# Performance work log

Hardware: AMD Instinct MI355X
Metric: run time of the kernel (lower is better)

## Reference

```python
import jax, jax.numpy as jnp
import numpy as np

NUM_ENT = 100000
NUM_REL = 50
NUM_EDGES = 200000
NNZ = 1000000
D = 128
BATCH = 4096
C = 1.0  # curvature k of the Lorentz manifold


def lorentz_linear(x, W, b, scale_param):
    # HyboNet-style LorentzLinear: linear map, then rescale so output lies on hyperboloid
    x = x @ W.T + b                                   # [N, D]
    time = jax.nn.sigmoid(x[..., :1]) * jnp.exp(scale_param) + 1.1   # [N, 1]
    xs = x[..., 1:]
    sqnorm = jnp.clip(jnp.sum(xs * xs, axis=-1, keepdims=True), 1e-8, None)
    s = jnp.sqrt((time * time - 1.0) / sqnorm)
    return jnp.concatenate([time, xs * s], axis=-1)


def logmap0(x, k):
    # Lorentz log map at the origin: time component -> 0, spatial rescaled by arccosh distance
    sqrtK = jnp.sqrt(jnp.asarray(k, x.dtype))
    y = x[..., 1:]
    y_norm = jnp.clip(jnp.linalg.norm(y, axis=-1, keepdims=True), 1e-8, None)
    theta = jnp.clip(x[..., :1] / sqrtK, 1.0 + 1e-7, None)
    spatial = sqrtK * jnp.arccosh(theta) * y / y_norm
    return jnp.concatenate([jnp.zeros_like(x[..., :1]), spatial], axis=-1)


def h2conv(X, emb_ty, vertex, edges, ty, lin_W, lin_b, lin_scale, eps):
    N = X.shape[0]
    Xl = lorentz_linear(X, lin_W, lin_b, lin_scale)           # [N, D]
    Xve = Xl[vertex] - emb_ty[ty]                             # [nnz, D] gather - relation translation
    Xe = jax.ops.segment_sum(Xve, edges, num_segments=NUM_EDGES)  # [E, D]
    Xev = Xe[edges]                                           # [nnz, D]
    Xv = jax.ops.segment_sum(Xev, vertex, num_segments=N)     # [N, D]
    return eps * Xv + Xl


def setup_inputs():
    key = jax.random.key(0)
    ks = jax.random.split(key, 20)
    n_ty = (NUM_REL - 1) * 6
    return {
        "emb_E": jax.random.normal(ks[0], (NUM_ENT, D), jnp.float32),
        "emb_R": jax.random.normal(ks[1], (NUM_REL, D), jnp.float32),
        "emb_ty": jax.random.normal(ks[2], (n_ty, D), jnp.float32),
        "lin_W": jax.random.normal(ks[3], (D, D), jnp.float32) * (1.0 / np.sqrt(D)),
        "lin_b": jnp.zeros((D,), jnp.float32),
        "lin_scale": jnp.asarray(np.log(10.0), jnp.float32),
        "eps": jnp.asarray([0.5], jnp.float32),
        "ms": jax.random.uniform(ks[4], (BATCH, 6), dtype=jnp.float32),
        "r_idx": jax.random.randint(ks[5], (BATCH,), 0, NUM_REL),
        "e1_idx": jax.random.randint(ks[6], (BATCH,), 0, NUM_ENT),
        "e2_idx": jax.random.randint(ks[7], (BATCH,), 0, NUM_ENT),
        "e3_idx": jax.random.randint(ks[8], (BATCH,), 0, NUM_ENT),
        "e4_idx": jax.random.randint(ks[9], (BATCH,), 0, NUM_ENT),
        "e5_idx": jax.random.randint(ks[10], (BATCH,), 0, NUM_ENT),
        "e6_idx": jax.random.randint(ks[11], (BATCH,), 0, NUM_ENT),
        "vertex": jax.random.randint(ks[12], (NNZ,), 0, NUM_ENT),
        "edges": jax.random.randint(ks[13], (NNZ,), 0, NUM_EDGES),
        "ty": jax.random.randint(ks[14], (NNZ,), 0, n_ty),
        "bs": BATCH,
    }


def reference(emb_E, emb_R, emb_ty, lin_W, lin_b, lin_scale, eps, ms,
              r_idx, e1_idx, e2_idx, e3_idx, e4_idx, e5_idx, e6_idx,
              vertex, edges, ty, bs):
    # (expmap0 result in the torch code is immediately overwritten, so omitted)
    E_e = h2conv(emb_E, emb_ty, vertex, edges, ty, lin_W, lin_b, lin_scale, eps)
    E_e = logmap0(E_e, C)
    E_e = E_e.at[0].set(1.0)
    R_e = emb_R.at[0].set(1.0)
    r = R_e[r_idx]
    x = (E_e[e1_idx] * E_e[e2_idx] * E_e[e3_idx] *
         E_e[e4_idx] * E_e[e5_idx] * E_e[e6_idx] * r)   # [B, D]
    return jnp.sum(x, axis=1)
```

## Files before the change

kernel.cpp:

```cpp
#include <hip/hip_runtime.h>
#include <math.h>

#define NUM_ENT   100000
#define NUM_REL   50
#define NUM_EDGES 200000
#define NNZ       1000000
#define DIM       128
#define BATCH     4096

#define CAP_E 32
#define CAP_V 40

#define XL_OFF  0
#define XH_OFF  (NUM_ENT * DIM)
#define XE_ROWS 150000
#define XE_OFF  (XH_OFF + NUM_ENT * DIM / 2)
#define INT_OFF (XE_OFF + XE_ROWS * DIM)

#define CUR_E   0
#define CUR_V   (CUR_E + NUM_EDGES)
#define BMV_O   (CUR_V + NUM_ENT)
#define FLAGE_O (BMV_O + 3136)
#define NV_CNT  (FLAGE_O + 50000)
#define NE_CNT  (NV_CNT + 1)
#define ZERO_N  (NE_CNT + 1)
#define VLIST   (ZERO_N)
#define ELIST   (VLIST + 24704)
#define EINV    (ELIST + NUM_EDGES)
#define PAYE    (EINV + NUM_EDGES)
#define PAYV    (PAYE + NUM_EDGES * CAP_E)
#define WSPHI   (PAYV + NUM_ENT * CAP_V)
#define WSPLO   (WSPHI + 8192)

#define FILL8_BLOCKS  489
#define ELIST4_BLOCKS 196
#define FLAGE8_BLOCKS 489
#define GEMM_TILES    1563
#define GF_GRID       2084

typedef __attribute__((ext_vector_type(8))) short sh8;
typedef __attribute__((ext_vector_type(4))) short sh4;
typedef __attribute__((ext_vector_type(4))) float f32x4;
typedef __attribute__((ext_vector_type(4))) _Float16 h4f;

__device__ __forceinline__ int bmtest(const unsigned* __restrict__ bm, int v) {
    return (bm[v >> 5] >> (v & 31)) & 1u;
}

__device__ __forceinline__ void split1(float x, unsigned short& h, unsigned short& l) {
    __bf16 hb = (__bf16)x;
    float hf = (float)hb;
    __bf16 lb = (__bf16)(x - hf);
    h = __builtin_bit_cast(unsigned short, hb);
    l = __builtin_bit_cast(unsigned short, lb);
}

__global__ __launch_bounds__(256, 4) void k_gemm_flage(const float* __restrict__ X,
                                                       const unsigned short* __restrict__ WhiG,
                                                       const unsigned short* __restrict__ WloG,
                                                       const float* __restrict__ bias,
                                                       const float* __restrict__ scale_p,
                                                       float* __restrict__ Y,
                                                       _Float16* __restrict__ Yh,
                                                       const unsigned* __restrict__ bmv,
                                                       const int* __restrict__ edges,
                                                       const int* __restrict__ vertex,
                                                       unsigned char* __restrict__ flag_e) {
    const int bid = blockIdx.x;
    const int sub = bid & 3, grp = bid >> 2;
    const int t = threadIdx.x;

    if (sub == 3) {
        if (grp >= FLAGE8_BLOCKS) return;
        int i8 = (grp * 256 + t) * 8;
        if (i8 >= NNZ) return;
        int4 v0 = *(const int4*)&vertex[i8];
        int4 v1 = *(const int4*)&vertex[i8 + 4];
        int4 e0 = *(const int4*)&edges[i8];
        int4 e1 = *(const int4*)&edges[i8 + 4];
        if (bmtest(bmv, v0.x)) flag_e[e0.x] = 1;
        if (bmtest(bmv, v0.y)) flag_e[e0.y] = 1;
        if (bmtest(bmv, v0.z)) flag_e[e0.z] = 1;
        if (bmtest(bmv, v0.w)) flag_e[e0.w] = 1;
        if (bmtest(bmv, v1.x)) flag_e[e1.x] = 1;
        if (bmtest(bmv, v1.y)) flag_e[e1.y] = 1;
        if (bmtest(bmv, v1.z)) flag_e[e1.z] = 1;
        if (bmtest(bmv, v1.w)) flag_e[e1.w] = 1;
        return;
    }

    __shared__ unsigned short Ahi[64 * 40], Alo[64 * 40];
    __shared__ unsigned short Bhi[128 * 40], Blo[128 * 40];
    __shared__ float biasS[128];

    const int tile = grp * 3 + sub;
    const int row0 = tile * 64;
    const int lane = t & 63, wv = t >> 6;
    const int cq = lane & 15, qd = lane >> 4;
    const float4* X4 = (const float4*)X;

    if (t < 128) biasS[t] = bias[t];

    f32x4 acc[8];
#pragma unroll
    for (int tn = 0; tn < 8; ++tn) acc[tn] = (f32x4){0.f, 0.f, 0.f, 0.f};

    for (int kc = 0; kc < 4; ++kc) {
#pragma unroll
        for (int i = 0; i < 2; ++i) {
            int q = t + 256 * i;
            int row = q >> 3, k4 = q & 7;
            int gr = row0 + row;
            float4 xv = make_float4(0.f, 0.f, 0.f, 0.f);
            if (gr < NUM_ENT) xv = X4[gr * 32 + kc * 8 + k4];
            unsigned short h0, h1, h2, h3, l0, l1, l2, l3;
            split1(xv.x, h0, l0); split1(xv.y, h1, l1);
            split1(xv.z, h2, l2); split1(xv.w, h3, l3);
            *(sh4*)&Ahi[row * 40 + k4 * 4] = (sh4){(short)h0, (short)h1, (short)h2, (short)h3};
            *(sh4*)&Alo[row * 40 + k4 * 4] = (sh4){(short)l0, (short)l1, (short)l2, (short)l3};
        }
#pragma unroll
        for (int i = 0; i < 4; ++i) {
            int q = t + 256 * i;
            int wr = q >> 3, k4 = q & 7;
            *(sh4*)&Bhi[wr * 40 + k4 * 4] =
                *(const sh4*)&WhiG[wr * 128 + kc * 32 + k4 * 4];
            *(sh4*)&Blo[wr * 40 + k4 * 4] =
                *(const sh4*)&WloG[wr * 128 + kc * 32 + k4 * 4];
        }
        __syncthreads();

        sh8 ah = *(const sh8*)&Ahi[(wv * 16 + cq) * 40 + qd * 8];
        sh8 al = *(const sh8*)&Alo[(wv * 16 + cq) * 40 + qd * 8];
#pragma unroll
        for (int tn = 0; tn < 8; ++tn) {
            sh8 bh = *(const sh8*)&Bhi[(tn * 16 + cq) * 40 + qd * 8];
            sh8 bl = *(const sh8*)&Blo[(tn * 16 + cq) * 40 + qd * 8];
            acc[tn] = __builtin_amdgcn_mfma_f32_16x16x32_bf16(ah, bh, acc[tn], 0, 0, 0);
            acc[tn] = __builtin_amdgcn_mfma_f32_16x16x32_bf16(ah, bl, acc[tn], 0, 0, 0);
            acc[tn] = __builtin_amdgcn_mfma_f32_16x16x32_bf16(al, bh, acc[tn], 0, 0, 0);
        }
        __syncthreads();
    }

    float es = expf(scale_p[0]);
    float psum[4] = {0.f, 0.f, 0.f, 0.f};
#pragma unroll
    for (int tn = 0; tn < 8; ++tn) {
        float bj = biasS[tn * 16 + cq];
#pragma unroll
        for (int reg = 0; reg < 4; ++reg) {
            float y = acc[tn][reg] + bj;
            acc[tn][reg] = y;
            psum[reg] += y * y;
        }
    }
#pragma unroll
    for (int off = 1; off < 16; off <<= 1) {
#pragma unroll
        for (int reg = 0; reg < 4; ++reg)
            psum[reg] += __shfl_xor(psum[reg], off, 64);
    }
    float srow[4], trow[4];
#pragma unroll
    for (int reg = 0; reg < 4; ++reg) {
        float y0 = __shfl(acc[0][reg], lane & 48, 64);
        float time = es / (1.f + expf(-y0)) + 1.1f;
        float ps = fmaxf(psum[reg] - y0 * y0, 1e-8f);
        srow[reg] = sqrtf((time * time - 1.f) / ps);
        trow[reg] = time;
    }
    int growv[4], fl[4];
#pragma unroll
    for (int reg = 0; reg < 4; ++reg) {
        int grow = row0 + wv * 16 + qd * 4 + reg;
        growv[reg] = grow;
        fl[reg] = (grow < NUM_ENT) ? bmtest(bmv, grow) : 0;
    }
#pragma unroll
    for (int tn = 0; tn < 8; ++tn) {
        int col = tn * 16 + cq;
#pragma unroll
        for (int reg = 0; reg < 4; ++reg) {
            if (growv[reg] < NUM_ENT) {
                float y = acc[tn][reg];
                float val = (col == 0) ? trow[reg] : y * srow[reg];
                Yh[growv[reg] * 128 + col] = (_Float16)val;
                if (fl[reg]) Y[growv[reg] * 128 + col] = val;
            }
        }
    }
}

__global__ __launch_bounds__(256) void k_flagv(const int* __restrict__ e1,
                                               const int* __restrict__ e2,
                                               const int* __restrict__ e3,
                                               const int* __restrict__ e4,
                                               const int* __restrict__ e5,
                                               const int* __restrict__ e6,
                                               unsigned* __restrict__ bmv,
                                               int* __restrict__ vlist,
                                               int* __restrict__ nv,
                                               const float* __restrict__ W,
                                               unsigned short* __restrict__ Whi,
                                               unsigned short* __restrict__ Wlo) {
    if (blockIdx.x >= 16) {
        int i = (blockIdx.x - 16) * 256 + threadIdx.x;
        unsigned short h, l;
        split1(W[i], h, l);
        Whi[i] = h; Wlo[i] = l;
        return;
    }
    int i = blockIdx.x * 256 + threadIdx.x;
    if (i >= BATCH) return;
    int idx[6] = {e1[i], e2[i], e3[i], e4[i], e5[i], e6[i]};
#pragma unroll
    for (int k = 0; k < 6; ++k) {
        int v = idx[k];
        unsigned bit = 1u << (v & 31);
        unsigned old = atomicOr(&bmv[v >> 5], bit);
        if (!(old & bit))
            vlist[atomicAdd(nv, 1)] = v;
    }
}

__global__ __launch_bounds__(256) void k_fill(const int* __restrict__ edges,
                                              const int* __restrict__ vertex,
                                              const int* __restrict__ tyi,
                                              const unsigned char* __restrict__ flag_e,
                                              const unsigned* __restrict__ bmv,
                                              int* __restrict__ cur_e,
                                              int* __restrict__ cur_v,
                                              int* __restrict__ pay_e,
                                              int* __restrict__ pay_v,
                                              int* __restrict__ elist,
                                              int* __restrict__ einv,
                                              int* __restrict__ ne) {
    int bid = blockIdx.x;
    if (bid >= FILL8_BLOCKS) {
        int i4 = ((bid - FILL8_BLOCKS) * 256 + threadIdx.x) * 4;
        if (i4 >= NUM_EDGES) return;
        int f[4], cnt = 0;
#pragma unroll
        for (int k = 0; k < 4; ++k) {
            int i = i4 + k;
            f[k] = (i < NUM_EDGES) ? flag_e[i] : 0;
            cnt += f[k];
        }
        if (cnt) {
            int g = atomicAdd(ne, cnt);
#pragma unroll
            for (int k = 0; k < 4; ++k) {
                if (f[k]) {
                    elist[g] = i4 + k;
                    einv[i4 + k] = g;
                    ++g;
                }
            }
        }
        return;
    }
    int i8 = (bid * 256 + threadIdx.x) * 8;
    if (i8 >= NNZ) return;
    int vv[8], ee[8], tt[8], nit;
    if (i8 + 7 < NNZ) {
        int4 v0 = *(const int4*)&vertex[i8];
        int4 v1 = *(const int4*)&vertex[i8 + 4];
        int4 e0 = *(const int4*)&edges[i8];
        int4 e1 = *(const int4*)&edges[i8 + 4];
        int4 t0 = *(const int4*)&tyi[i8];
        int4 t1 = *(const int4*)&tyi[i8 + 4];
        vv[0] = v0.x; vv[1] = v0.y; vv[2] = v0.z; vv[3] = v0.w;
        vv[4] = v1.x; vv[5] = v1.y; vv[6] = v1.z; vv[7] = v1.w;
        ee[0] = e0.x; ee[1] = e0.y; ee[2] = e0.z; ee[3] = e0.w;
        ee[4] = e1.x; ee[5] = e1.y; ee[6] = e1.z; ee[7] = e1.w;
        tt[0] = t0.x; tt[1] = t0.y; tt[2] = t0.z; tt[3] = t0.w;
        tt[4] = t1.x; tt[5] = t1.y; tt[6] = t1.z; tt[7] = t1.w;
        nit = 8;
    } else {
        nit = NNZ - i8;
        for (int k = 0; k < nit; ++k) {
            vv[k] = vertex[i8 + k]; ee[k] = edges[i8 + k]; tt[k] = tyi[i8 + k];
        }
    }
#pragma unroll 8
    for (int k = 0; k < nit; ++k) {
        int v = vv[k], e = ee[k];
        if (flag_e[e]) {
            int p = atomicAdd(&cur_e[e], 1);
            if (p < CAP_E) pay_e[e * CAP_E + p] = (v << 9) | tt[k];
        }
        if (bmtest(bmv, v)) {
            int q = atomicAdd(&cur_v[v], 1);
            if (q < CAP_V) pay_v[v * CAP_V + q] = e;
        }
    }
}

__global__ __launch_bounds__(256) void k_gatherE(const _Float16* __restrict__ Xlh,
                                                 const float* __restrict__ Ty,
                                                 const int* __restrict__ elist,
                                                 const int* __restrict__ ne_p,
                                                 const int* __restrict__ cur_e,
                                                 const int* __restrict__ pay_e,
                                                 float* __restrict__ Xe) {
    int tid = blockIdx.x * 256 + threadIdx.x;
    int g = tid >> 5, l = tid & 31;
    if (g >= ne_p[0] || g >= XE_ROWS) return;
    int e = elist[g];
    int n = cur_e[e]; n = (n > CAP_E) ? CAP_E : n;
    int myPay = pay_e[e * CAP_E + l];
    const int base = threadIdx.x & 32;
    const h4f* Xh4 = (const h4f*)Xlh;
    const float4* Ty4 = (const float4*)Ty;
    float4 acc = make_float4(0.f, 0.f, 0.f, 0.f);
    int k = 0;
    for (; k + 4 <= n; k += 4) {
        int pe0 = __shfl(myPay, base + k,     64);
        int pe1 = __shfl(myPay, base + k + 1, 64);
        int pe2 = __shfl(myPay, base + k + 2, 64);
        int pe3 = __shfl(myPay, base + k + 3, 64);
        h4f a0 = Xh4[(pe0 >> 9) * 32 + l];
        h4f a1 = Xh4[(pe1 >> 9) * 32 + l];
        h4f a2 = Xh4[(pe2 >> 9) * 32 + l];
        h4f a3 = Xh4[(pe3 >> 9) * 32 + l];
        float4 c0 = Ty4[(pe0 & 511) * 32 + l];
        float4 c1 = Ty4[(pe1 & 511) * 32 + l];
        float4 c2 = Ty4[(pe2 & 511) * 32 + l];
        float4 c3 = Ty4[(pe3 & 511) * 32 + l];
        acc.x += (float)a0.x - c0.x; acc.y += (float)a0.y - c0.y;
        acc.z += (float)a0.z - c0.z; acc.w += (float)a0.w - c0.w;
        acc.x += (float)a1.x - c1.x; acc.y += (float)a1.y - c1.y;
        acc.z += (float)a1.z - c1.z; acc.w += (float)a1.w - c1.w;
        acc.x += (float)a2.x - c2.x; acc.y += (float)a2.y - c2.y;
        acc.z += (float)a2.z - c2.z; acc.w += (float)a2.w - c2.w;
        acc.x += (float)a3.x - c3.x; acc.y += (float)a3.y - c3.y;
        acc.z += (float)a3.z - c3.z; acc.w += (float)a3.w - c3.w;
    }
    for (; k < n; ++k) {
        int pe = __shfl(myPay, base + k, 64);
        int v = pe >> 9, tt = pe & 511;
        h4f a = Xh4[v * 32 + l];
        float4 c = Ty4[tt * 32 + l];
        acc.x += (float)a.x - c.x; acc.y += (float)a.y - c.y;
        acc.z += (float)a.z - c.z; acc.w += (float)a.w - c.w;
    }
    ((float4*)Xe)[g * 32 + l] = acc;
}

__global__ __launch_bounds__(256) void k_gatherV_final(float* __restrict__ XlEe,
                                                       const float* __restrict__ Xe,
                                                       const int* __restrict__ cur_v,
                                                       const int* __restrict__ pay_v,
                                                       const int* __restrict__ einv,
                                                       const int* __restrict__ vlist,
                                                       const int* __restrict__ nv_p,
                                                       const float* __restrict__ eps_p) {
    int gid = blockIdx.x * 256 + threadIdx.x;
    int idx = gid >> 6, lane = gid & 63;
    if (idx >= nv_p[0]) return;
    int w = vlist[idx];
    int n = cur_v[w]; n = (n > CAP_V) ? CAP_V : n;
    int pidx = (lane < CAP_V) ? lane : (CAP_V - 1);
    int myE = pay_v[w * CAP_V + pidx];
    myE = (pidx < n) ? myE : 0;
    int myG = einv[myE];
    float base_a = XlEe[w * 128 + lane];
    float base_b = XlEe[w * 128 + 64 + lane];
    float sa = 0.f, sb = 0.f;
    int k = 0;
    for (; k + 4 <= n; k += 4) {
        int g0 = __shfl(myG, k,     64);
        int g1 = __shfl(myG, k + 1, 64);
        int g2 = __shfl(myG, k + 2, 64);
        int g3 = __shfl(myG, k + 3, 64);
        float a0 = Xe[g0 * 128 + lane],      a1 = Xe[g1 * 128 + lane];
        float a2 = Xe[g2 * 128 + lane],      a3 = Xe[g3 * 128 + lane];
        float b0 = Xe[g0 * 128 + 64 + lane], b1 = Xe[g1 * 128 + 64 + lane];
        float b2 = Xe[g2 * 128 + 64 + lane], b3 = Xe[g3 * 128 + 64 + lane];
        sa += a0 + a1 + a2 + a3;
        sb += b0 + b1 + b2 + b3;
    }
    for (; k < n; ++k) {
        int g = __shfl(myG, k, 64);
        sa += Xe[g * 128 + lane];
        sb += Xe[g * 128 + 64 + lane];
    }
    float eps = eps_p[0];
    float xa = fmaf(eps, sa, base_a);
    float xb = fmaf(eps, sb, base_b);
    float x0 = __shfl(xa, 0, 64);
    float sq = xa * xa + xb * xb;
#pragma unroll
    for (int off = 32; off > 0; off >>= 1) sq += __shfl_xor(sq, off, 64);
    sq = fmaxf(sq - x0 * x0, 0.f);
    float ynorm = fmaxf(sqrtf(sq), 1e-8f);
    float theta = fmaxf(x0, 1.f + 1e-7f);
    float fac = logf(theta + sqrtf(theta * theta - 1.f)) / ynorm;
    float oa = (lane == 0) ? 0.f : xa * fac;
    float ob = xb * fac;
    if (w == 0) { oa = 1.f; ob = 1.f; }
    XlEe[w * 128 + lane]      = oa;
    XlEe[w * 128 + 64 + lane] = ob;
}

__global__ __launch_bounds__(256) void k_out(const float* __restrict__ Ee,
                                             const float* __restrict__ R,
                                             const int* __restrict__ r_idx,
                                             const int* __restrict__ e1,
                                             const int* __restrict__ e2,
                                             const int* __restrict__ e3,
                                             const int* __restrict__ e4,
                                             const int* __restrict__ e5,
                                             const int* __restrict__ e6,
                                             float* __restrict__ out) {
    int gid = blockIdx.x * 256 + threadIdx.x;
    int b = gid >> 6, lane = gid & 63;
    if (b >= BATCH) return;
    int i1 = e1[b], i2 = e2[b], i3 = e3[b], i4 = e4[b], i5 = e5[b], i6 = e6[b];
    int rr = r_idx[b];
    float pa = Ee[i1 * 128 + lane] * Ee[i2 * 128 + lane] * Ee[i3 * 128 + lane]
             * Ee[i4 * 128 + lane] * Ee[i5 * 128 + lane] * Ee[i6 * 128 + lane];
    float pb = Ee[i1 * 128 + 64 + lane] * Ee[i2 * 128 + 64 + lane] * Ee[i3 * 128 + 64 + lane]
             * Ee[i4 * 128 + 64 + lane] * Ee[i5 * 128 + 64 + lane] * Ee[i6 * 128 + 64 + lane];
    float ra = (rr == 0) ? 1.f : R[rr * 128 + lane];
    float rb = (rr == 0) ? 1.f : R[rr * 128 + 64 + lane];
    float s = pa * ra + pb * rb;
#pragma unroll
    for (int off = 32; off > 0; off >>= 1) s += __shfl_xor(s, off, 64);
    if (lane == 0) out[b] = s;
}

extern "C" void kernel_launch(void* const* d_in, const int* in_sizes, int n_in,
                              void* d_out, int out_size, void* d_ws, size_t ws_size,
                              hipStream_t stream) {
    const float* emb_E     = (const float*)d_in[0];
    const float* emb_R     = (const float*)d_in[1];
    const float* emb_ty    = (const float*)d_in[2];
    const float* lin_W     = (const float*)d_in[3];
    const float* lin_b     = (const float*)d_in[4];
    const float* lin_scale = (const float*)d_in[5];
    const float* eps       = (const float*)d_in[6];
    const int* r_idx  = (const int*)d_in[8];
    const int* e1     = (const int*)d_in[9];
    const int* e2     = (const int*)d_in[10];
    const int* e3     = (const int*)d_in[11];
    const int* e4     = (const int*)d_in[12];
    const int* e5     = (const int*)d_in[13];
    const int* e6     = (const int*)d_in[14];
    const int* vertex = (const int*)d_in[15];
    const int* edges  = (const int*)d_in[16];
    const int* tyi    = (const int*)d_in[17];

    float* ws = (float*)d_ws;
    float* Xl = ws + XL_OFF;
    _Float16* Xlh = (_Float16*)(ws + XH_OFF);
    float* Xe = ws + XE_OFF;
    int*   ib = (int*)(ws + INT_OFF);
    int* cur_e  = ib + CUR_E;
    int* cur_v  = ib + CUR_V;
    unsigned* bmv = (unsigned*)(ib + BMV_O);
    unsigned char* flag_e = (unsigned char*)(ib + FLAGE_O);
    int* nv     = ib + NV_CNT;
    int* ne     = ib + NE_CNT;
    int* vlist  = ib + VLIST;
    int* elist  = ib + ELIST;
    int* einv   = ib + EINV;
    int* pay_e  = ib + PAYE;
    int* pay_v  = ib + PAYV;
    unsigned short* Whi = (unsigned short*)(ib + WSPHI);
    unsigned short* Wlo = (unsigned short*)(ib + WSPLO);

    hipMemsetAsync(cur_e, 0, (size_t)ZERO_N * sizeof(int), stream);

    k_flagv<<<16 + 64, 256, 0, stream>>>(e1, e2, e3, e4, e5, e6,
                                         bmv, vlist, nv,
                                         lin_W, Whi, Wlo);

    k_gemm_flage<<<GF_GRID, 256, 0, stream>>>(emb_E, Whi, Wlo, lin_b,
                                              lin_scale, Xl, Xlh, bmv,
                                              edges, vertex, flag_e);

    k_fill<<<FILL8_BLOCKS + ELIST4_BLOCKS, 256, 0, stream>>>(edges, vertex, tyi,
                                                             flag_e, bmv,
                                                             cur_e, cur_v,
                                                             pay_e, pay_v,
                                                             elist, einv, ne);

    k_gatherE<<<(NUM_EDGES * 32) / 256, 256, 0, stream>>>(Xlh, emb_ty, elist, ne,
                                                          cur_e, pay_e, Xe);
    k_gatherV_final<<<(BATCH * 6 * 64) / 256, 256, 0, stream>>>(Xl, Xe, cur_v,
                                                                pay_v, einv,
                                                                vlist, nv, eps);
    k_out<<<(BATCH * 64) / 256, 256, 0, stream>>>(Xl, emb_R, r_idx,
                                                  e1, e2, e3, e4, e5, e6,
                                                  (float*)d_out);
}
```

Measured before the change: 306.0 us.

## Split flag-edge pass from GEMM and store edge sums in half precision

```diff
diff --git a/kernel.cpp b/kernel.cpp
--- a/kernel.cpp
+++ b/kernel.cpp
@@ -16,7 +16,6 @@
 #define XE_ROWS 150000
 #define XE_OFF  (XH_OFF + NUM_ENT * DIM / 2)
 #define INT_OFF (XE_OFF + XE_ROWS * DIM)
-
 #define CUR_E   0
 #define CUR_V   (CUR_E + NUM_EDGES)
 #define BMV_O   (CUR_V + NUM_ENT)
@@ -35,8 +34,6 @@
 #define FILL8_BLOCKS  489
 #define ELIST4_BLOCKS 196
 #define FLAGE8_BLOCKS 489
-#define GEMM_TILES    1563
-#define GF_GRID       2084
 
 typedef __attribute__((ext_vector_type(8))) short sh8;
 typedef __attribute__((ext_vector_type(4))) short sh4;
@@ -55,46 +52,20 @@
     l = __builtin_bit_cast(unsigned short, lb);
 }
 
-__global__ __launch_bounds__(256, 4) void k_gemm_flage(const float* __restrict__ X,
-                                                       const unsigned short* __restrict__ WhiG,
-                                                       const unsigned short* __restrict__ WloG,
-                                                       const float* __restrict__ bias,
-                                                       const float* __restrict__ scale_p,
-                                                       float* __restrict__ Y,
-                                                       _Float16* __restrict__ Yh,
-                                                       const unsigned* __restrict__ bmv,
-                                                       const int* __restrict__ edges,
-                                                       const int* __restrict__ vertex,
-                                                       unsigned char* __restrict__ flag_e) {
-    const int bid = blockIdx.x;
-    const int sub = bid & 3, grp = bid >> 2;
-    const int t = threadIdx.x;
-
-    if (sub == 3) {
-        if (grp >= FLAGE8_BLOCKS) return;
-        int i8 = (grp * 256 + t) * 8;
-        if (i8 >= NNZ) return;
-        int4 v0 = *(const int4*)&vertex[i8];
-        int4 v1 = *(const int4*)&vertex[i8 + 4];
-        int4 e0 = *(const int4*)&edges[i8];
-        int4 e1 = *(const int4*)&edges[i8 + 4];
-        if (bmtest(bmv, v0.x)) flag_e[e0.x] = 1;
-        if (bmtest(bmv, v0.y)) flag_e[e0.y] = 1;
-        if (bmtest(bmv, v0.z)) flag_e[e0.z] = 1;
-        if (bmtest(bmv, v0.w)) flag_e[e0.w] = 1;
-        if (bmtest(bmv, v1.x)) flag_e[e1.x] = 1;
-        if (bmtest(bmv, v1.y)) flag_e[e1.y] = 1;
-        if (bmtest(bmv, v1.z)) flag_e[e1.z] = 1;
-        if (bmtest(bmv, v1.w)) flag_e[e1.w] = 1;
-        return;
-    }
-
+__global__ __launch_bounds__(256, 4) void k_gemm_lorentz(const float* __restrict__ X,
+                                                         const unsigned short* __restrict__ WhiG,
+                                                         const unsigned short* __restrict__ WloG,
+                                                         const float* __restrict__ bias,
+                                                         const float* __restrict__ scale_p,
+                                                         float* __restrict__ Y,
+                                                         _Float16* __restrict__ Yh,
+                                                         const unsigned* __restrict__ bmv) {
     __shared__ unsigned short Ahi[64 * 40], Alo[64 * 40];
     __shared__ unsigned short Bhi[128 * 40], Blo[128 * 40];
     __shared__ float biasS[128];
 
-    const int tile = grp * 3 + sub;
-    const int row0 = tile * 64;
+    const int t = threadIdx.x;
+    const int row0 = blockIdx.x * 64;
     const int lane = t & 63, wv = t >> 6;
     const int cq = lane & 15, qd = lane >> 4;
     const float4* X4 = (const float4*)X;
@@ -222,6 +193,26 @@
         if (!(old & bit))
             vlist[atomicAdd(nv, 1)] = v;
     }
+}
+
+__global__ __launch_bounds__(256) void k_flage(const int* __restrict__ edges,
+                                               const int* __restrict__ vertex,
+                                               const unsigned* __restrict__ bmv,
+                                               unsigned char* __restrict__ flag_e) {
+    int i8 = (blockIdx.x * 256 + threadIdx.x) * 8;
+    if (i8 >= NNZ) return;
+    int4 v0 = *(const int4*)&vertex[i8];
+    int4 v1 = *(const int4*)&vertex[i8 + 4];
+    int4 e0 = *(const int4*)&edges[i8];
+    int4 e1 = *(const int4*)&edges[i8 + 4];
+    if (bmtest(bmv, v0.x)) flag_e[e0.x] = 1;
+    if (bmtest(bmv, v0.y)) flag_e[e0.y] = 1;
+    if (bmtest(bmv, v0.z)) flag_e[e0.z] = 1;
+    if (bmtest(bmv, v0.w)) flag_e[e0.w] = 1;
+    if (bmtest(bmv, v1.x)) flag_e[e1.x] = 1;
+    if (bmtest(bmv, v1.y)) flag_e[e1.y] = 1;
+    if (bmtest(bmv, v1.z)) flag_e[e1.z] = 1;
+    if (bmtest(bmv, v1.w)) flag_e[e1.w] = 1;
 }
 
 __global__ __launch_bounds__(256) void k_fill(const int* __restrict__ edges,
@@ -303,7 +294,7 @@
                                                  const int* __restrict__ ne_p,
                                                  const int* __restrict__ cur_e,
                                                  const int* __restrict__ pay_e,
-                                                 float* __restrict__ Xe) {
+                                                 _Float16* __restrict__ Xe) {
     int tid = blockIdx.x * 256 + threadIdx.x;
     int g = tid >> 5, l = tid & 31;
     if (g >= ne_p[0] || g >= XE_ROWS) return;
@@ -345,11 +336,12 @@
         acc.x += (float)a.x - c.x; acc.y += (float)a.y - c.y;
         acc.z += (float)a.z - c.z; acc.w += (float)a.w - c.w;
     }
-    ((float4*)Xe)[g * 32 + l] = acc;
+    h4f o = {(_Float16)acc.x, (_Float16)acc.y, (_Float16)acc.z, (_Float16)acc.w};
+    ((h4f*)Xe)[g * 32 + l] = o;
 }
 
 __global__ __launch_bounds__(256) void k_gatherV_final(float* __restrict__ XlEe,
-                                                       const float* __restrict__ Xe,
+                                                       const _Float16* __restrict__ Xe,
                                                        const int* __restrict__ cur_v,
                                                        const int* __restrict__ pay_v,
                                                        const int* __restrict__ einv,
@@ -374,17 +366,17 @@
         int g1 = __shfl(myG, k + 1, 64);
         int g2 = __shfl(myG, k + 2, 64);
         int g3 = __shfl(myG, k + 3, 64);
-        float a0 = Xe[g0 * 128 + lane],      a1 = Xe[g1 * 128 + lane];
-        float a2 = Xe[g2 * 128 + lane],      a3 = Xe[g3 * 128 + lane];
-        float b0 = Xe[g0 * 128 + 64 + lane], b1 = Xe[g1 * 128 + 64 + lane];
-        float b2 = Xe[g2 * 128 + 64 + lane], b3 = Xe[g3 * 128 + 64 + lane];
+        float a0 = (float)Xe[g0 * 128 + lane],      a1 = (float)Xe[g1 * 128 + lane];
+        float a2 = (float)Xe[g2 * 128 + lane],      a3 = (float)Xe[g3 * 128 + lane];
+        float b0 = (float)Xe[g0 * 128 + 64 + lane], b1 = (float)Xe[g1 * 128 + 64 + lane];
+        float b2 = (float)Xe[g2 * 128 + 64 + lane], b3 = (float)Xe[g3 * 128 + 64 + lane];
         sa += a0 + a1 + a2 + a3;
         sb += b0 + b1 + b2 + b3;
     }
     for (; k < n; ++k) {
         int g = __shfl(myG, k, 64);
-        sa += Xe[g * 128 + lane];
-        sb += Xe[g * 128 + 64 + lane];
+        sa += (float)Xe[g * 128 + lane];
+        sb += (float)Xe[g * 128 + 64 + lane];
     }
     float eps = eps_p[0];
     float xa = fmaf(eps, sa, base_a);
@@ -455,7 +447,7 @@
     float* ws = (float*)d_ws;
     float* Xl = ws + XL_OFF;
     _Float16* Xlh = (_Float16*)(ws + XH_OFF);
-    float* Xe = ws + XE_OFF;
+    _Float16* Xe = (_Float16*)(ws + XE_OFF);
     int*   ib = (int*)(ws + INT_OFF);
     int* cur_e  = ib + CUR_E;
     int* cur_v  = ib + CUR_V;
@@ -476,17 +468,16 @@
     k_flagv<<<16 + 64, 256, 0, stream>>>(e1, e2, e3, e4, e5, e6,
                                          bmv, vlist, nv,
                                          lin_W, Whi, Wlo);
-
-    k_gemm_flage<<<GF_GRID, 256, 0, stream>>>(emb_E, Whi, Wlo, lin_b,
-                                              lin_scale, Xl, Xlh, bmv,
-                                              edges, vertex, flag_e);
-
+    k_flage<<<FLAGE8_BLOCKS, 256, 0, stream>>>(edges, vertex, bmv, flag_e);
     k_fill<<<FILL8_BLOCKS + ELIST4_BLOCKS, 256, 0, stream>>>(edges, vertex, tyi,
                                                              flag_e, bmv,
                                                              cur_e, cur_v,
                                                              pay_e, pay_v,
                                                              elist, einv, ne);
 
+    k_gemm_lorentz<<<(NUM_ENT + 63) / 64, 256, 0, stream>>>(emb_E, Whi, Wlo, lin_b,
+                                                            lin_scale, Xl, Xlh,
+                                                            bmv);
     k_gatherE<<<(NUM_EDGES * 32) / 256, 256, 0, stream>>>(Xlh, emb_ty, elist, ne,
                                                           cur_e, pay_e, Xe);
     k_gatherV_final<<<(BATCH * 6 * 64) / 256, 256, 0, stream>>>(Xl, Xe, cur_v,
```

Result: faster. 285.8 us (-6.6%).
